# Optimization experiments

Hardware: AMD Instinct MI355X
Metric: run time of the kernel (lower is better)

Reference implementation:

```python
import jax, jax.numpy as jnp
import numpy as np

EPS = 1e-8  # torch.cosine_similarity default eps (applied per-norm clamp)


def setup_inputs() -> dict:
    key = jax.random.key(0)
    k1, k2, k3 = jax.random.split(key, 3)
    B, D = 8192, 4096
    ques = jax.random.normal(k1, (B, D), dtype=jnp.float32)
    ans = jax.random.normal(k2, (B, D), dtype=jnp.float32)
    # labels in {-1, +1}, shape [B, 1] as in the torch module
    label = (2 * jax.random.randint(k3, (B, 1), 0, 2) - 1).astype(jnp.int32)
    margin = 0.5  # scalar hinge margin
    return {"ques": ques, "ans": ans, "label": label, "margin": margin}


def reference(ques, ans, label, margin):
    # Per-row cosine similarity (torch semantics: each norm clamped to eps)
    qn = jnp.maximum(jnp.linalg.norm(ques, axis=-1), EPS)  # [B]
    an = jnp.maximum(jnp.linalg.norm(ans, axis=-1), EPS)   # [B]
    cos = jnp.sum(ques * ans, axis=-1) / (qn * an)          # [B]

    lab = label[:, 0]
    mask_true = lab == 1
    mask_false = lab == -1

    true_ave = jnp.sum(jnp.where(mask_true, cos, 0.0)) / jnp.sum(mask_true)
    false_ave = jnp.sum(jnp.where(mask_false, cos, 0.0)) / jnp.sum(mask_false)

    loss = jnp.maximum(0.0, margin - true_ave + false_ave)
    return loss.reshape(1)  # torch version returns a shape-[1] tensor
```

## Files before the change

kernel.cpp:

```cpp
#include <hip/hip_runtime.h>

#define D_DIM 4096
#define EPSF 1e-8f

typedef float f32x4 __attribute__((ext_vector_type(4)));

__global__ __launch_bounds__(256) void cosim_rows(const float* __restrict__ q,
                                                  const float* __restrict__ a,
                                                  float* __restrict__ cosv) {
    const int row  = (blockIdx.x * 256 + threadIdx.x) >> 6;
    const int lane = threadIdx.x & 63;

    const f32x4* q4 = reinterpret_cast<const f32x4*>(q + (size_t)row * D_DIM);
    const f32x4* a4 = reinterpret_cast<const f32x4*>(a + (size_t)row * D_DIM);

    float dot = 0.f, qq = 0.f, aa = 0.f;
#pragma unroll
    for (int k = 0; k < 16; ++k) {
        f32x4 vq = q4[lane + k * 64];
        f32x4 va = a4[lane + k * 64];
        dot += vq.x * va.x + vq.y * va.y + vq.z * va.z + vq.w * va.w;
        qq  += vq.x * vq.x + vq.y * vq.y + vq.z * vq.z + vq.w * vq.w;
        aa  += va.x * va.x + va.y * va.y + va.z * va.z + va.w * va.w;
    }

#pragma unroll
    for (int off = 32; off > 0; off >>= 1) {
        dot += __shfl_down(dot, off, 64);
        qq  += __shfl_down(qq,  off, 64);
        aa  += __shfl_down(aa,  off, 64);
    }

    if (lane == 0) {
        float qn = fmaxf(sqrtf(qq), EPSF);
        float an = fmaxf(sqrtf(aa), EPSF);
        cosv[row] = dot / (qn * an);
    }
}

__global__ __launch_bounds__(256) void cosim_finalize(const float* __restrict__ cosv,
                                                      const int* __restrict__ label,
                                                      const float* __restrict__ margin,
                                                      float* __restrict__ out, int B) {
    const int t = threadIdx.x;
    float ts = 0.f, fs = 0.f, tc = 0.f, fc = 0.f;
    for (int i = t; i < B; i += 256) {
        float c = cosv[i];
        int l = label[i];
        if (l == 1)       { ts += c; tc += 1.f; }
        else if (l == -1) { fs += c; fc += 1.f; }
    }
#pragma unroll
    for (int off = 32; off > 0; off >>= 1) {
        ts += __shfl_down(ts, off, 64);
        fs += __shfl_down(fs, off, 64);
        tc += __shfl_down(tc, off, 64);
        fc += __shfl_down(fc, off, 64);
    }
    __shared__ float s[4][4];
    const int wave = t >> 6;
    if ((t & 63) == 0) { s[0][wave] = ts; s[1][wave] = fs; s[2][wave] = tc; s[3][wave] = fc; }
    __syncthreads();
    if (t == 0) {
        float tsum = s[0][0] + s[0][1] + s[0][2] + s[0][3];
        float fsum = s[1][0] + s[1][1] + s[1][2] + s[1][3];
        float tcnt = s[2][0] + s[2][1] + s[2][2] + s[2][3];
        float fcnt = s[3][0] + s[3][1] + s[3][2] + s[3][3];
        out[0] = fmaxf(0.f, margin[0] - tsum / tcnt + fsum / fcnt);
    }
}

extern "C" void kernel_launch(void* const* d_in, const int* in_sizes, int n_in,
                              void* d_out, int out_size, void* d_ws, size_t ws_size,
                              hipStream_t stream) {
    const float* ques   = (const float*)d_in[0];
    const float* ans    = (const float*)d_in[1];
    const int*   label  = (const int*)d_in[2];
    const float* margin = (const float*)d_in[3];
    float* out = (float*)d_out;

    const int B = in_sizes[2];
    float* cosv = (float*)d_ws;

    cosim_rows<<<B / 4, 256, 0, stream>>>(ques, ans, cosv);
    cosim_finalize<<<1, 256, 0, stream>>>(cosv, label, margin, out, B);
}
```

Measured before the change: 61.69 us.

## Fuse finalize into row kernel via binned atomics and last-block reduction

Merges the per-row cosine kernel and the single-block finalize kernel into one launch. Each block reduces its four rows' masked sums and counts, atomically adds them into one of 64 bins, and the last block to bump a counter reduces the bins and writes the loss. This removes the second kernel launch and the intermediate cosine vector, at the cost of a memset launch, global atomics, and reliance on an inline-asm dependency trick to order the counter increment after the bin updates.

After: 59.86 us. -3.0%, faster.

```diff
diff --git a/kernel.cpp b/kernel.cpp
--- a/kernel.cpp
+++ b/kernel.cpp
@@ -2,14 +2,24 @@
 
 #define D_DIM 4096
 #define EPSF 1e-8f
+#define NBINS 64
 
 typedef float f32x4 __attribute__((ext_vector_type(4)));
 
-__global__ __launch_bounds__(256) void cosim_rows(const float* __restrict__ q,
-                                                  const float* __restrict__ a,
-                                                  float* __restrict__ cosv) {
-    const int row  = (blockIdx.x * 256 + threadIdx.x) >> 6;
-    const int lane = threadIdx.x & 63;
+__global__ __launch_bounds__(256) void cosim_fused(const float* __restrict__ q,
+                                                   const float* __restrict__ a,
+                                                   const int* __restrict__ label,
+                                                   const float* __restrict__ margin,
+                                                   float* __restrict__ tbin,
+                                                   float* __restrict__ fbin,
+                                                   unsigned* __restrict__ tcb,
+                                                   unsigned* __restrict__ fcb,
+                                                   unsigned* __restrict__ counter,
+                                                   float* __restrict__ out) {
+    const int t    = threadIdx.x;
+    const int lane = t & 63;
+    const int wave = t >> 6;
+    const int row  = blockIdx.x * 4 + wave;
 
     const f32x4* q4 = reinterpret_cast<const f32x4*>(q + (size_t)row * D_DIM);
     const f32x4* a4 = reinterpret_cast<const f32x4*>(a + (size_t)row * D_DIM);
@@ -31,42 +41,61 @@
         aa  += __shfl_down(aa,  off, 64);
     }
 
+    __shared__ float    sh_t[4], sh_f[4];
+    __shared__ unsigned sh_tc[4], sh_fc[4];
+    __shared__ unsigned sh_prev;
+
     if (lane == 0) {
         float qn = fmaxf(sqrtf(qq), EPSF);
         float an = fmaxf(sqrtf(aa), EPSF);
-        cosv[row] = dot / (qn * an);
+        float c  = dot / (qn * an);
+        int l = label[row];
+        sh_t[wave]  = (l == 1)  ? c : 0.f;
+        sh_f[wave]  = (l == -1) ? c : 0.f;
+        sh_tc[wave] = (l == 1)  ? 1u : 0u;
+        sh_fc[wave] = (l == -1) ? 1u : 0u;
     }
-}
+    __syncthreads();
 
-__global__ __launch_bounds__(256) void cosim_finalize(const float* __restrict__ cosv,
-                                                      const int* __restrict__ label,
-                                                      const float* __restrict__ margin,
-                                                      float* __restrict__ out, int B) {
-    const int t = threadIdx.x;
-    float ts = 0.f, fs = 0.f, tc = 0.f, fc = 0.f;
-    for (int i = t; i < B; i += 256) {
-        float c = cosv[i];
-        int l = label[i];
-        if (l == 1)       { ts += c; tc += 1.f; }
-        else if (l == -1) { fs += c; fc += 1.f; }
+    if (t == 0) {
+        float    ts = sh_t[0] + sh_t[1] + sh_t[2] + sh_t[3];
+        float    fs = sh_f[0] + sh_f[1] + sh_f[2] + sh_f[3];
+        unsigned tc = sh_tc[0] + sh_tc[1] + sh_tc[2] + sh_tc[3];
+        unsigned fc = sh_fc[0] + sh_fc[1] + sh_fc[2] + sh_fc[3];
+        const int b = blockIdx.x & (NBINS - 1);
+        float    o1 = atomicAdd(&tbin[b], ts);
+        float    o2 = atomicAdd(&fbin[b], fs);
+        unsigned o3 = atomicAdd(&tcb[b], tc);
+        unsigned o4 = atomicAdd(&fcb[b], fc);
+        unsigned dep = __float_as_uint(o1) | __float_as_uint(o2) | o3 | o4;
+        asm volatile("v_and_b32 %0, 0, %0" : "+v"(dep));
+        sh_prev = atomicAdd(counter, 1u + dep);
     }
+    __syncthreads();
+
+    if (sh_prev == (unsigned)(gridDim.x - 1)) {
+        float    tb = 0.f, fb = 0.f;
+        unsigned tcv = 0u, fcv = 0u;
+        if (t < NBINS) {
+            tb  = atomicAdd(&tbin[t], 0.f);
+            fb  = atomicAdd(&fbin[t], 0.f);
+            tcv = atomicAdd(&tcb[t], 0u);
+            fcv = atomicAdd(&fcb[t], 0u);
+        }
+        if (wave == 0) {
 #pragma unroll
-    for (int off = 32; off > 0; off >>= 1) {
-        ts += __shfl_down(ts, off, 64);
-        fs += __shfl_down(fs, off, 64);
-        tc += __shfl_down(tc, off, 64);
-        fc += __shfl_down(fc, off, 64);
-    }
-    __shared__ float s[4][4];
-    const int wave = t >> 6;
-    if ((t & 63) == 0) { s[0][wave] = ts; s[1][wave] = fs; s[2][wave] = tc; s[3][wave] = fc; }
-    __syncthreads();
-    if (t == 0) {
-        float tsum = s[0][0] + s[0][1] + s[0][2] + s[0][3];
-        float fsum = s[1][0] + s[1][1] + s[1][2] + s[1][3];
-        float tcnt = s[2][0] + s[2][1] + s[2][2] + s[2][3];
-        float fcnt = s[3][0] + s[3][1] + s[3][2] + s[3][3];
-        out[0] = fmaxf(0.f, margin[0] - tsum / tcnt + fsum / fcnt);
+            for (int off = 32; off > 0; off >>= 1) {
+                tb  += __shfl_down(tb,  off, 64);
+                fb  += __shfl_down(fb,  off, 64);
+                tcv += __shfl_down(tcv, off, 64);
+                fcv += __shfl_down(fcv, off, 64);
+            }
+            if (t == 0) {
+                float true_ave  = tb / (float)tcv;
+                float false_ave = fb / (float)fcv;
+                out[0] = fmaxf(0.f, margin[0] - true_ave + false_ave);
+            }
+        }
     }
 }
 
@@ -80,8 +109,13 @@
     float* out = (float*)d_out;
 
     const int B = in_sizes[2];
-    float* cosv = (float*)d_ws;
+    float*    tbin    = (float*)d_ws;
+    float*    fbin    = (float*)((char*)d_ws + 256);
+    unsigned* tcb     = (unsigned*)((char*)d_ws + 512);
+    unsigned* fcb     = (unsigned*)((char*)d_ws + 768);
+    unsigned* counter = (unsigned*)((char*)d_ws + 1024);
 
-    cosim_rows<<<B / 4, 256, 0, stream>>>(ques, ans, cosv);
-    cosim_finalize<<<1, 256, 0, stream>>>(cosv, label, margin, out, B);
+    hipMemsetAsync(d_ws, 0, 1056, stream);
+    cosim_fused<<<B / 4, 256, 0, stream>>>(ques, ans, label, margin,
+                                           tbin, fbin, tcb, fcb, counter, out);
 }
```
